# Optimization experiments

Measured on AMD Instinct MI355X. Metric: run time of the kernel, lower is better.

## Reference

```python
import jax, jax.numpy as jnp
import numpy as np

EPS = 1e-5

@jax.custom_vjp
def spike(u):
    return (u >= 0).astype(u.dtype)

def _spike_fwd(u):
    return spike(u), u

def _spike_bwd(u, g):
    return (g / (1.0 + 5.0 * jnp.abs(u)) ** 2,)

spike.defvjp(_spike_fwd, _spike_bwd)


def setup_inputs() -> dict:
    key = jax.random.key(0)
    ks = jax.random.split(key, 20)
    B, T, IN, TH, H = 2048, 320, 64, 128, 64
    d = {}
    d['x'] = jax.random.normal(ks[0], (B, T, IN), jnp.float32)
    d['tda'] = jax.random.normal(ks[1], (B, 150), jnp.float32)
    # depthwise conv: Conv1d(64,128,k=15,pad=7,groups=64) -> kernel [128, 1, 15]
    d['conv_w'] = jax.random.normal(ks[2], (TH, 1, 15), jnp.float32) * 0.1
    d['conv_b'] = jnp.zeros((TH,), jnp.float32)
    d['bn1_g'] = jnp.ones((TH,), jnp.float32)
    d['bn1_b'] = jnp.zeros((TH,), jnp.float32)
    d['bn1_m'] = jnp.zeros((TH,), jnp.float32)
    d['bn1_v'] = jnp.ones((TH,), jnp.float32)
    # spatial_fc: Linear(128,64), init mean=0.05 std=0.1
    d['sp_w'] = 0.05 + 0.1 * jax.random.normal(ks[3], (H, TH), jnp.float32)
    d['sp_b'] = jnp.zeros((H,), jnp.float32)
    d['li_w'] = jax.random.normal(ks[4], (H, 2 * H), jnp.float32) * (1.0 / np.sqrt(2 * H))
    d['li_b'] = jnp.zeros((H,), jnp.float32)
    d['tda_w1'] = jax.random.normal(ks[5], (64, 150), jnp.float32) * (1.0 / np.sqrt(150))
    d['tda_b1'] = jnp.zeros((64,), jnp.float32)
    d['tda_w2'] = jax.random.normal(ks[6], (32, 64), jnp.float32) * 0.125
    d['tda_b2'] = jnp.zeros((32,), jnp.float32)
    dp_out = (320 // 32) * H  # 640
    d['cls_w1'] = jax.random.normal(ks[7], (128, dp_out + 32), jnp.float32) * (1.0 / np.sqrt(dp_out + 32))
    d['cls_b1'] = jnp.zeros((128,), jnp.float32)
    d['bn2_g'] = jnp.ones((128,), jnp.float32)
    d['bn2_b'] = jnp.zeros((128,), jnp.float32)
    d['bn2_m'] = jnp.zeros((128,), jnp.float32)
    d['bn2_v'] = jnp.ones((128,), jnp.float32)
    d['cls_w2'] = jax.random.normal(ks[8], (4, 128), jnp.float32) * (1.0 / np.sqrt(128))
    d['cls_b2'] = jnp.zeros((4,), jnp.float32)
    return d


def reference(x, tda, conv_w, conv_b, bn1_g, bn1_b, bn1_m, bn1_v, sp_w, sp_b,
              li_w, li_b, tda_w1, tda_b1, tda_w2, tda_b2,
              cls_w1, cls_b1, bn2_g, bn2_b, bn2_m, bn2_v, cls_w2, cls_b2):
    B, T, _ = x.shape
    L_DP, N_DP, H = 32, 16, 64
    # temp_conv (eval mode: no dropout, BN with running stats)
    xc = jnp.transpose(x, (0, 2, 1))  # [B, 64, T]
    y = jax.lax.conv_general_dilated(
        xc, conv_w, window_strides=(1,), padding=[(7, 7)],
        dimension_numbers=('NCH', 'OIH', 'NCH'), feature_group_count=64)
    y = y + conv_b[None, :, None]
    y = (y - bn1_m[None, :, None]) * jax.lax.rsqrt(bn1_v + EPS)[None, :, None] * bn1_g[None, :, None] + bn1_b[None, :, None]
    y = jax.nn.relu(y)
    y = jnp.transpose(y, (0, 2, 1))  # [B, T, 128]
    # precompute all input currents: [T, B, 64] (time-major for scan)
    cur_all = jnp.einsum('bth,oh->tbo', y, sp_w) + sp_b

    def step(carry, cur):
        mf, ms, ml = carry
        mf = 0.5 * mf + cur
        sf = spike(mf - 0.5)
        mf = mf * (1.0 - sf)
        ms = 0.9 * ms + cur
        ss = spike(ms - 1.0)
        ms = ms * (1.0 - ss)
        cur_li = jnp.concatenate([sf, ss], axis=-1) @ li_w.T + li_b
        ml = 0.9 * ml + cur_li
        return (mf, ms, ml), ml

    z0 = jnp.zeros((B, H), x.dtype)
    _, li_seq = jax.lax.scan(step, (z0, z0, z0), cur_all)  # [T, B, 64]
    li_seq = jnp.transpose(li_seq, (1, 0, 2))  # [B, T, 64]

    windows = li_seq.reshape(B, T // L_DP, L_DP, H)
    start_mean = windows[:, :, :N_DP, :].mean(axis=2)
    end_mean = windows[:, :, -N_DP:, :].mean(axis=2)
    dp_feat = (end_mean - start_mean).reshape(B, -1)  # [B, 640]

    t1 = jax.nn.relu(tda @ tda_w1.T + tda_b1)
    tda_feat = jax.nn.relu(t1 @ tda_w2.T + tda_b2)  # [B, 32]

    h = jnp.concatenate([dp_feat, tda_feat], axis=-1) @ cls_w1.T + cls_b1
    h = (h - bn2_m) * jax.lax.rsqrt(bn2_v + EPS) * bn2_g + bn2_b
    h = jax.nn.relu(h)
    return h @ cls_w2.T + cls_b2  # [B, 4]
```

## Files before the change

### kernel.cpp

```cpp
#include <hip/hip_runtime.h>

#define NT 256

#define WS_SPWT    0
#define WS_SC1     8192
#define WS_SH1     8320
#define WS_SC2     8448
#define WS_SH2     8576
#define WS_LIWT    8704
#define WS_TW1T    16896
#define WS_TW2T    26496
#define WS_CW1T    28544
#define WS_TOTAL   114560
#define WS_WG      114560
#define WS_WBASE   114688
#define WS_CURBASE (114688 + 2048*1280)
#define CUR_STRIDE 20480

__global__ void prep_kernel(
    const float* __restrict__ conv_b, const float* __restrict__ bn1_g,
    const float* __restrict__ bn1_b,  const float* __restrict__ bn1_m,
    const float* __restrict__ bn1_v,  const float* __restrict__ sp_w,
    const float* __restrict__ li_w,   const float* __restrict__ tda_w1,
    const float* __restrict__ tda_w2, const float* __restrict__ cls_w1,
    const float* __restrict__ bn2_g,  const float* __restrict__ bn2_b,
    const float* __restrict__ bn2_m,  const float* __restrict__ bn2_v,
    float* __restrict__ ws)
{
    int i = blockIdx.x * NT + threadIdx.x;
    if (i > WS_TOTAL) return;
    if (i == WS_TOTAL) {
        float g = 0.f, sE = 0.f, sL = 0.f; int w = 0;
        for (int t = 0; t < 320; ++t) {
            g = fmaf(0.9f, g, 1.f);
            int pos = t & 31;
            if (pos < 16) sE += g; else sL += g;
            if (pos == 31) { ws[WS_WG + w] = sL - sE; ++w; sE = 0.f; sL = 0.f; }
        }
        return;
    }
    if (i < WS_SC1) {
        int c = i >> 6, h = i & 63;
        ws[i] = sp_w[h*128 + c];
    } else if (i < WS_SH1) {
        int c = i - WS_SC1;
        float vv = bn1_v[c] + 1e-5f;
        ws[i] = (float)((double)bn1_g[c] / sqrt((double)vv));
    } else if (i < WS_SC2) {
        int c = i - WS_SH1;
        float vv = bn1_v[c] + 1e-5f;
        double s = (double)bn1_g[c] / sqrt((double)vv);
        ws[i] = (float)(((double)conv_b[c] - (double)bn1_m[c])*s + (double)bn1_b[c]);
    } else if (i < WS_SH2) {
        int c = i - WS_SC2;
        float vv = bn2_v[c] + 1e-5f;
        ws[i] = (float)((double)bn2_g[c] / sqrt((double)vv));
    } else if (i < WS_LIWT) {
        int c = i - WS_SH2;
        float vv = bn2_v[c] + 1e-5f;
        double s = (double)bn2_g[c] / sqrt((double)vv);
        ws[i] = (float)((double)bn2_b[c] - (double)bn2_m[c]*s);
    } else if (i < WS_TW1T) {
        int t = i - WS_LIWT; int j = t >> 6, o = t & 63;
        ws[i] = li_w[o*128 + j];
    } else if (i < WS_TW2T) {
        int t = i - WS_TW1T; int r = t >> 6, o = t & 63;
        ws[i] = tda_w1[o*150 + r];
    } else if (i < WS_CW1T) {
        int t = i - WS_TW2T; int j = t >> 5, o = t & 31;
        ws[i] = tda_w2[o*64 + j];
    } else {
        int t = i - WS_CW1T; int j = t >> 7, c = t & 127;
        ws[i] = cls_w1[c*672 + j];
    }
}

__launch_bounds__(NT, 4)
__global__ void convproj_kernel(
    const float* __restrict__ x, const float* __restrict__ conv_w,
    const float* __restrict__ sp_b, const float* __restrict__ ws,
    float* __restrict__ cur, int b0)
{
    __shared__ float y_lds[128*65];

    const int tid = threadIdx.x;
    const int bi  = blockIdx.x;
    const int ic  = tid & 63;
    const int tg  = tid >> 6;
    const int lane = tid & 63;
    const int h0 = __builtin_amdgcn_readfirstlane((tid >> 6) << 4);

    float w0[15], w1[15];
    #pragma unroll
    for (int k = 0; k < 15; ++k) {
        w0[k] = conv_w[(2*ic)*15 + k];
        w1[k] = conv_w[(2*ic + 1)*15 + k];
    }
    const float sA = ws[WS_SC1 + 2*ic],     hA = ws[WS_SH1 + 2*ic];
    const float sB = ws[WS_SC1 + 2*ic + 1], hB = ws[WS_SH1 + 2*ic + 1];
    const float4* bp = reinterpret_cast<const float4*>(sp_b + h0);
    const float4 b0v = bp[0], b1v = bp[1], b2v = bp[2], b3v = bp[3];

    const float* __restrict__ spwT = ws;
    const float* xb = x + (size_t)(b0 + bi) * 20480 + ic;
    float* curb = cur + (size_t)bi * CUR_STRIDE;

    float xr0[30], xr1[30];
    #pragma unroll
    for (int r = 0; r < 30; ++r) {
        int t = tg*16 - 7 + r;
        xr0[r] = (t >= 0) ? xb[(size_t)t * 64] : 0.f;
    }

    #pragma unroll
    for (int chk = 0; chk < 5; ++chk) {
        float* xc = (chk & 1) ? xr1 : xr0;
        float* xn = (chk & 1) ? xr0 : xr1;

        #pragma unroll
        for (int j = 0; j < 16; ++j) {
            float a0 = 0.f, a1 = 0.f;
            #pragma unroll
            for (int k = 0; k < 15; ++k) {
                a0 = fmaf(xc[j + k], w0[k], a0);
                a1 = fmaf(xc[j + k], w1[k], a1);
            }
            int tt = tg*16 + j;
            y_lds[(2*ic)*65 + tt]     = fmaxf(fmaf(a0, sA, hA), 0.f);
            y_lds[(2*ic + 1)*65 + tt] = fmaxf(fmaf(a1, sB, hB), 0.f);
        }
        __syncthreads();

        if (chk < 4) {
            const int tbase = (chk + 1)*64 + tg*16 - 7;
            if (tbase + 29 < 320) {
                #pragma unroll
                for (int r = 0; r < 30; ++r)
                    xn[r] = xb[(size_t)(tbase + r) * 64];
            } else {
                #pragma unroll
                for (int r = 0; r < 30; ++r) {
                    int t = tbase + r;
                    xn[r] = (t < 320) ? xb[(size_t)t * 64] : 0.f;
                }
            }
        }

        {
            float acc[16];
            acc[0]=b0v.x;  acc[1]=b0v.y;  acc[2]=b0v.z;  acc[3]=b0v.w;
            acc[4]=b1v.x;  acc[5]=b1v.y;  acc[6]=b1v.z;  acc[7]=b1v.w;
            acc[8]=b2v.x;  acc[9]=b2v.y;  acc[10]=b2v.z; acc[11]=b2v.w;
            acc[12]=b3v.x; acc[13]=b3v.y; acc[14]=b3v.z; acc[15]=b3v.w;

            #pragma unroll 4
            for (int c = 0; c < 128; ++c) {
                float yv = y_lds[c*65 + lane];
                const float4* wp = reinterpret_cast<const float4*>(spwT + c*64 + h0);
                float4 q0 = wp[0], q1 = wp[1], q2 = wp[2], q3 = wp[3];
                acc[0]  = fmaf(yv, q0.x, acc[0]);
                acc[1]  = fmaf(yv, q0.y, acc[1]);
                acc[2]  = fmaf(yv, q0.z, acc[2]);
                acc[3]  = fmaf(yv, q0.w, acc[3]);
                acc[4]  = fmaf(yv, q1.x, acc[4]);
                acc[5]  = fmaf(yv, q1.y, acc[5]);
                acc[6]  = fmaf(yv, q1.z, acc[6]);
                acc[7]  = fmaf(yv, q1.w, acc[7]);
                acc[8]  = fmaf(yv, q2.x, acc[8]);
                acc[9]  = fmaf(yv, q2.y, acc[9]);
                acc[10] = fmaf(yv, q2.z, acc[10]);
                acc[11] = fmaf(yv, q2.w, acc[11]);
                acc[12] = fmaf(yv, q3.x, acc[12]);
                acc[13] = fmaf(yv, q3.y, acc[13]);
                acc[14] = fmaf(yv, q3.z, acc[14]);
                acc[15] = fmaf(yv, q3.w, acc[15]);
            }
            float* cb = curb + (size_t)h0 * 320 + chk*64 + lane;
            #pragma unroll
            for (int j = 0; j < 16; ++j)
                cb[(size_t)j*320] = acc[j];
        }
        __syncthreads();
    }
}

__device__ __forceinline__ void lif16(float4 n0, float4 n1, float4 n2, float4 n3,
    float& mf, float& ms, float& rlo, float& rhi,
    float& slo, float& shi)
{
    float v[16] = {n0.x,n0.y,n0.z,n0.w, n1.x,n1.y,n1.z,n1.w,
                   n2.x,n2.y,n2.z,n2.w, n3.x,n3.y,n3.z,n3.w};
    slo = 0.f; shi = 0.f;
    #pragma unroll
    for (int q = 0; q < 16; ++q) {
        float c = v[q];
        mf = fmaf(0.5f, mf, c);
        bool sf = mf >= 0.5f;
        ms = fmaf(0.9f, ms, c);
        bool ss = ms >= 1.0f;
        mf = sf ? 0.f : mf;
        ms = ss ? 0.f : ms;
        rlo = fmaf(0.9f, rlo, sf ? 1.f : 0.f);
        rhi = fmaf(0.9f, rhi, ss ? 1.f : 0.f);
        slo += rlo; shi += rhi;
    }
}

__global__ void scan_kernel(const float* __restrict__ cur,
                            float* __restrict__ W, int b0, int nb)
{
    const int wv = (int)((blockIdx.x * (unsigned)blockDim.x + threadIdx.x) >> 6);
    if (wv >= nb) return;
    const int lane = threadIdx.x & 63;
    const float* cb = cur + (size_t)wv * CUR_STRIDE + (size_t)lane * 320;
    float* Wb = W + (size_t)(b0 + wv) * 1280;

    float mf = 0.f, ms = 0.f, rlo = 0.f, rhi = 0.f;

    float4 A0 = *reinterpret_cast<const float4*>(cb);
    float4 A1 = *reinterpret_cast<const float4*>(cb + 4);
    float4 A2 = *reinterpret_cast<const float4*>(cb + 8);
    float4 A3 = *reinterpret_cast<const float4*>(cb + 12);
    float4 B0 = *reinterpret_cast<const float4*>(cb + 16);
    float4 B1 = *reinterpret_cast<const float4*>(cb + 20);
    float4 B2 = *reinterpret_cast<const float4*>(cb + 24);
    float4 B3 = *reinterpret_cast<const float4*>(cb + 28);

    #pragma unroll 1
    for (int tb = 0; tb < 20; tb += 2) {
        float sE_lo, sE_hi, slo, shi;
        lif16(A0, A1, A2, A3, mf, ms, rlo, rhi, sE_lo, sE_hi);
        if (tb + 2 < 20) {
            const float* p = cb + (tb + 2) * 16;
            A0 = *reinterpret_cast<const float4*>(p);
            A1 = *reinterpret_cast<const float4*>(p + 4);
            A2 = *reinterpret_cast<const float4*>(p + 8);
            A3 = *reinterpret_cast<const float4*>(p + 12);
        }
        lif16(B0, B1, B2, B3, mf, ms, rlo, rhi, slo, shi);
        if (tb + 3 < 20) {
            const float* p = cb + (tb + 3) * 16;
            B0 = *reinterpret_cast<const float4*>(p);
            B1 = *reinterpret_cast<const float4*>(p + 4);
            B2 = *reinterpret_cast<const float4*>(p + 8);
            B3 = *reinterpret_cast<const float4*>(p + 12);
        }
        int wdx = tb >> 1;
        Wb[wdx*128 + lane]      = slo - sE_lo;
        Wb[wdx*128 + 64 + lane] = shi - sE_hi;
    }
}

__global__ void epilogue_kernel(
    const float* __restrict__ tda,    const float* __restrict__ li_b,
    const float* __restrict__ tda_b1, const float* __restrict__ tda_b2,
    const float* __restrict__ cls_b1, const float* __restrict__ cls_w2,
    const float* __restrict__ cls_b2, const float* __restrict__ ws,
    const float* __restrict__ W,      float* __restrict__ out)
{
    __shared__ float Wl[1280];
    __shared__ float t1[64], tf[32], dp[640], h1[128];
    const int b = blockIdx.x, tid = threadIdx.x;

    for (int i = tid; i < 1280; i += NT)
        Wl[i] = W[(size_t)b*1280 + i];
    __syncthreads();

    const float* __restrict__ liwT = ws + WS_LIWT;
    const float* __restrict__ tw1T = ws + WS_TW1T;
    const float* __restrict__ tw2T = ws + WS_TW2T;
    const float* __restrict__ cw1T = ws + WS_CW1T;
    const float* tdab = tda + b*150;

    if (tid < 64) {
        float acc = tda_b1[tid];
        for (int i2 = 0; i2 < 150; ++i2)
            acc = fmaf(tdab[i2], tw1T[i2*64 + tid], acc);
        t1[tid] = fmaxf(acc, 0.f);
    }
    __syncthreads();
    if (tid < 32) {
        float acc = tda_b2[tid];
        #pragma unroll 8
        for (int j = 0; j < 64; ++j)
            acc = fmaf(t1[j], tw2T[j*32 + tid], acc);
        tf[tid] = fmaxf(acc, 0.f);
    }
    {
        int o = tid & 63;
        for (int w = tid >> 6; w < 10; w += 4) {
            float acc = li_b[o] * ws[WS_WG + w];
            #pragma unroll 4
            for (int j = 0; j < 128; ++j)
                acc = fmaf(Wl[w*128 + j], liwT[j*64 + o], acc);
            dp[w*64 + o] = 0.0625f * acc;
        }
    }
    __syncthreads();
    if (tid < 128) {
        float acc = cls_b1[tid];
        for (int j = 0; j < 640; ++j)
            acc = fmaf(dp[j], cw1T[j*128 + tid], acc);
        #pragma unroll 4
        for (int j = 0; j < 32; ++j)
            acc = fmaf(tf[j], cw1T[(640 + j)*128 + tid], acc);
        float s2 = ws[WS_SC2 + tid], sh2 = ws[WS_SH2 + tid];
        h1[tid] = fmaxf(fmaf(acc, s2, sh2), 0.f);
    }
    __syncthreads();
    if (tid < 4) {
        float acc = cls_b2[tid];
        for (int c = 0; c < 128; ++c)
            acc = fmaf(h1[c], cls_w2[tid*128 + c], acc);
        out[b*4 + tid] = acc;
    }
}

extern "C" void kernel_launch(void* const* d_in, const int* in_sizes, int n_in,
                              void* d_out, int out_size, void* d_ws, size_t ws_size,
                              hipStream_t stream) {
    const float* x      = (const float*)d_in[0];
    const float* tda    = (const float*)d_in[1];
    const float* conv_w = (const float*)d_in[2];
    const float* conv_b = (const float*)d_in[3];
    const float* bn1_g  = (const float*)d_in[4];
    const float* bn1_b  = (const float*)d_in[5];
    const float* bn1_m  = (const float*)d_in[6];
    const float* bn1_v  = (const float*)d_in[7];
    const float* sp_w   = (const float*)d_in[8];
    const float* sp_b   = (const float*)d_in[9];
    const float* li_w   = (const float*)d_in[10];
    const float* li_b   = (const float*)d_in[11];
    const float* tda_w1 = (const float*)d_in[12];
    const float* tda_b1 = (const float*)d_in[13];
    const float* tda_w2 = (const float*)d_in[14];
    const float* tda_b2 = (const float*)d_in[15];
    const float* cls_w1 = (const float*)d_in[16];
    const float* cls_b1 = (const float*)d_in[17];
    const float* bn2_g  = (const float*)d_in[18];
    const float* bn2_b  = (const float*)d_in[19];
    const float* bn2_m  = (const float*)d_in[20];
    const float* bn2_v  = (const float*)d_in[21];
    const float* cls_w2 = (const float*)d_in[22];
    const float* cls_b2 = (const float*)d_in[23];
    float* ws  = (float*)d_ws;
    float* out = (float*)d_out;

    const int B = in_sizes[0] / (320 * 64);

    prep_kernel<<<(WS_TOTAL + 1 + NT - 1)/NT, NT, 0, stream>>>(
        conv_b, bn1_g, bn1_b, bn1_m, bn1_v, sp_w,
        li_w, tda_w1, tda_w2, cls_w1,
        bn2_g, bn2_b, bn2_m, bn2_v, ws);

    long cap = (long)(ws_size / 4) - (long)WS_CURBASE;
    int nbg = (int)(cap / CUR_STRIDE);
    if (nbg < 1) nbg = 1;
    if (nbg > B) nbg = B;

    for (int g0 = 0; g0 < B; g0 += nbg) {
        int nb = (B - g0 < nbg) ? (B - g0) : nbg;
        convproj_kernel<<<nb, NT, 0, stream>>>(
            x, conv_w, sp_b, ws, ws + WS_CURBASE, g0);
        scan_kernel<<<(nb + 3)/4, NT, 0, stream>>>(
            ws + WS_CURBASE, ws + WS_WBASE, g0, nb);
    }

    epilogue_kernel<<<B, NT, 0, stream>>>(
        tda, li_b, tda_b1, tda_b2, cls_b1, cls_w2, cls_b2,
        ws, ws + WS_WBASE, out);
}
```

Before: 289.9 us.

## Fuse conv-projection and LIF scan into one kernel via LDS staging

Merges the conv/projection kernel and the scan kernel into a single per-batch kernel. Spatial currents are staged through a swizzled LDS buffer instead of a global workspace, and one wavefront runs the LIF recurrence on each 64-step chunk. The conv for the next chunk is reordered so the other waves can compute it while that wavefront scans. This removes the global round trip of the current tensor and the batch-group launch loop. The costs are more LDS per block, lower occupancy (launch bounds lowered from 4 to 3) and a serial scan on one wave inside the block, which may leave the other waves idle at the barrier.

Result: faster. 249.7 us (-13.8%).

```diff
diff --git a/kernel.cpp b/kernel.cpp
--- a/kernel.cpp
+++ b/kernel.cpp
@@ -14,8 +14,6 @@
 #define WS_TOTAL   114560
 #define WS_WG      114560
 #define WS_WBASE   114688
-#define WS_CURBASE (114688 + 2048*1280)
-#define CUR_STRIDE 20480
 
 __global__ void prep_kernel(
     const float* __restrict__ conv_b, const float* __restrict__ bn1_g,
@@ -75,20 +73,21 @@
     }
 }
 
-__launch_bounds__(NT, 4)
-__global__ void convproj_kernel(
+__launch_bounds__(NT, 3)
+__global__ void fused_kernel(
     const float* __restrict__ x, const float* __restrict__ conv_w,
     const float* __restrict__ sp_b, const float* __restrict__ ws,
-    float* __restrict__ cur, int b0)
+    float* __restrict__ wfeat)
 {
     __shared__ float y_lds[128*65];
-
-    const int tid = threadIdx.x;
-    const int bi  = blockIdx.x;
-    const int ic  = tid & 63;
-    const int tg  = tid >> 6;
+    __shared__ float cur_lds[64*64];
+
+    const int tid  = threadIdx.x;
+    const int b    = blockIdx.x;
+    const int ic   = tid & 63;
+    const int tg   = tid >> 6;
     const int lane = tid & 63;
-    const int h0 = __builtin_amdgcn_readfirstlane((tid >> 6) << 4);
+    const int h0   = __builtin_amdgcn_readfirstlane((tid >> 6) << 4);
 
     float w0[15], w1[15];
     #pragma unroll
@@ -102,8 +101,10 @@
     const float4 b0v = bp[0], b1v = bp[1], b2v = bp[2], b3v = bp[3];
 
     const float* __restrict__ spwT = ws;
-    const float* xb = x + (size_t)(b0 + bi) * 20480 + ic;
-    float* curb = cur + (size_t)bi * CUR_STRIDE;
+    const float* xb = x + (size_t)b * 20480 + ic;
+    float* Wb = wfeat + (size_t)b * 1280;
+
+    float mf = 0.f, ms = 0.f, rlo = 0.f, rhi = 0.f;
 
     float xr0[30], xr1[30];
     #pragma unroll
@@ -111,25 +112,23 @@
         int t = tg*16 - 7 + r;
         xr0[r] = (t >= 0) ? xb[(size_t)t * 64] : 0.f;
     }
+    #pragma unroll
+    for (int j = 0; j < 16; ++j) {
+        float a0 = 0.f, a1 = 0.f;
+        #pragma unroll
+        for (int k = 0; k < 15; ++k) {
+            a0 = fmaf(xr0[j + k], w0[k], a0);
+            a1 = fmaf(xr0[j + k], w1[k], a1);
+        }
+        int tt = tg*16 + j;
+        y_lds[(2*ic)*65 + tt]     = fmaxf(fmaf(a0, sA, hA), 0.f);
+        y_lds[(2*ic + 1)*65 + tt] = fmaxf(fmaf(a1, sB, hB), 0.f);
+    }
+    __syncthreads();
 
     #pragma unroll
     for (int chk = 0; chk < 5; ++chk) {
-        float* xc = (chk & 1) ? xr1 : xr0;
         float* xn = (chk & 1) ? xr0 : xr1;
-
-        #pragma unroll
-        for (int j = 0; j < 16; ++j) {
-            float a0 = 0.f, a1 = 0.f;
-            #pragma unroll
-            for (int k = 0; k < 15; ++k) {
-                a0 = fmaf(xc[j + k], w0[k], a0);
-                a1 = fmaf(xc[j + k], w1[k], a1);
-            }
-            int tt = tg*16 + j;
-            y_lds[(2*ic)*65 + tt]     = fmaxf(fmaf(a0, sA, hA), 0.f);
-            y_lds[(2*ic + 1)*65 + tt] = fmaxf(fmaf(a1, sB, hB), 0.f);
-        }
-        __syncthreads();
 
         if (chk < 4) {
             const int tbase = (chk + 1)*64 + tg*16 - 7;
@@ -175,79 +174,63 @@
                 acc[14] = fmaf(yv, q3.z, acc[14]);
                 acc[15] = fmaf(yv, q3.w, acc[15]);
             }
-            float* cb = curb + (size_t)h0 * 320 + chk*64 + lane;
+            const int tsw = (lane & 15) << 2;
             #pragma unroll
-            for (int j = 0; j < 16; ++j)
-                cb[(size_t)j*320] = acc[j];
+            for (int k = 0; k < 4; ++k) {
+                float4 v4 = make_float4(acc[4*k], acc[4*k+1], acc[4*k+2], acc[4*k+3]);
+                *reinterpret_cast<float4*>(&cur_lds[lane*64 + ((h0 + 4*k) ^ tsw)]) = v4;
+            }
         }
         __syncthreads();
-    }
-}
-
-__device__ __forceinline__ void lif16(float4 n0, float4 n1, float4 n2, float4 n3,
-    float& mf, float& ms, float& rlo, float& rhi,
-    float& slo, float& shi)
-{
-    float v[16] = {n0.x,n0.y,n0.z,n0.w, n1.x,n1.y,n1.z,n1.w,
-                   n2.x,n2.y,n2.z,n2.w, n3.x,n3.y,n3.z,n3.w};
-    slo = 0.f; shi = 0.f;
-    #pragma unroll
-    for (int q = 0; q < 16; ++q) {
-        float c = v[q];
-        mf = fmaf(0.5f, mf, c);
-        bool sf = mf >= 0.5f;
-        ms = fmaf(0.9f, ms, c);
-        bool ss = ms >= 1.0f;
-        mf = sf ? 0.f : mf;
-        ms = ss ? 0.f : ms;
-        rlo = fmaf(0.9f, rlo, sf ? 1.f : 0.f);
-        rhi = fmaf(0.9f, rhi, ss ? 1.f : 0.f);
-        slo += rlo; shi += rhi;
-    }
-}
-
-__global__ void scan_kernel(const float* __restrict__ cur,
-                            float* __restrict__ W, int b0, int nb)
-{
-    const int wv = (int)((blockIdx.x * (unsigned)blockDim.x + threadIdx.x) >> 6);
-    if (wv >= nb) return;
-    const int lane = threadIdx.x & 63;
-    const float* cb = cur + (size_t)wv * CUR_STRIDE + (size_t)lane * 320;
-    float* Wb = W + (size_t)(b0 + wv) * 1280;
-
-    float mf = 0.f, ms = 0.f, rlo = 0.f, rhi = 0.f;
-
-    float4 A0 = *reinterpret_cast<const float4*>(cb);
-    float4 A1 = *reinterpret_cast<const float4*>(cb + 4);
-    float4 A2 = *reinterpret_cast<const float4*>(cb + 8);
-    float4 A3 = *reinterpret_cast<const float4*>(cb + 12);
-    float4 B0 = *reinterpret_cast<const float4*>(cb + 16);
-    float4 B1 = *reinterpret_cast<const float4*>(cb + 20);
-    float4 B2 = *reinterpret_cast<const float4*>(cb + 24);
-    float4 B3 = *reinterpret_cast<const float4*>(cb + 28);
-
-    #pragma unroll 1
-    for (int tb = 0; tb < 20; tb += 2) {
-        float sE_lo, sE_hi, slo, shi;
-        lif16(A0, A1, A2, A3, mf, ms, rlo, rhi, sE_lo, sE_hi);
-        if (tb + 2 < 20) {
-            const float* p = cb + (tb + 2) * 16;
-            A0 = *reinterpret_cast<const float4*>(p);
-            A1 = *reinterpret_cast<const float4*>(p + 4);
-            A2 = *reinterpret_cast<const float4*>(p + 8);
-            A3 = *reinterpret_cast<const float4*>(p + 12);
-        }
-        lif16(B0, B1, B2, B3, mf, ms, rlo, rhi, slo, shi);
-        if (tb + 3 < 20) {
-            const float* p = cb + (tb + 3) * 16;
-            B0 = *reinterpret_cast<const float4*>(p);
-            B1 = *reinterpret_cast<const float4*>(p + 4);
-            B2 = *reinterpret_cast<const float4*>(p + 8);
-            B3 = *reinterpret_cast<const float4*>(p + 12);
-        }
-        int wdx = tb >> 1;
-        Wb[wdx*128 + lane]      = slo - sE_lo;
-        Wb[wdx*128 + 64 + lane] = shi - sE_hi;
+
+        if (tid < 64) {
+            float sE_lo = 0.f, sE_hi = 0.f;
+            #pragma unroll
+            for (int gq = 0; gq < 4; ++gq) {
+                float v[16];
+                #pragma unroll
+                for (int q = 0; q < 16; ++q) {
+                    int t = gq*16 + q;
+                    v[q] = cur_lds[t*64 + (lane ^ ((t & 15) << 2))];
+                }
+                float slo = 0.f, shi = 0.f;
+                #pragma unroll
+                for (int q = 0; q < 16; ++q) {
+                    float c = v[q];
+                    mf = fmaf(0.5f, mf, c);
+                    bool sf = mf >= 0.5f;
+                    ms = fmaf(0.9f, ms, c);
+                    bool ss = ms >= 1.0f;
+                    mf = sf ? 0.f : mf;
+                    ms = ss ? 0.f : ms;
+                    rlo = fmaf(0.9f, rlo, sf ? 1.f : 0.f);
+                    rhi = fmaf(0.9f, rhi, ss ? 1.f : 0.f);
+                    slo += rlo; shi += rhi;
+                }
+                if ((gq & 1) == 0) {
+                    sE_lo = slo; sE_hi = shi;
+                } else {
+                    int wdx = chk*2 + (gq >> 1);
+                    Wb[wdx*128 + lane]      = slo - sE_lo;
+                    Wb[wdx*128 + 64 + lane] = shi - sE_hi;
+                }
+            }
+        }
+        if (chk < 4) {
+            #pragma unroll
+            for (int j = 0; j < 16; ++j) {
+                float a0 = 0.f, a1 = 0.f;
+                #pragma unroll
+                for (int k = 0; k < 15; ++k) {
+                    a0 = fmaf(xn[j + k], w0[k], a0);
+                    a1 = fmaf(xn[j + k], w1[k], a1);
+                }
+                int tt = tg*16 + j;
+                y_lds[(2*ic)*65 + tt]     = fmaxf(fmaf(a0, sA, hA), 0.f);
+                y_lds[(2*ic + 1)*65 + tt] = fmaxf(fmaf(a1, sB, hB), 0.f);
+            }
+        }
+        __syncthreads();
     }
 }
 
@@ -353,18 +336,8 @@
         li_w, tda_w1, tda_w2, cls_w1,
         bn2_g, bn2_b, bn2_m, bn2_v, ws);
 
-    long cap = (long)(ws_size / 4) - (long)WS_CURBASE;
-    int nbg = (int)(cap / CUR_STRIDE);
-    if (nbg < 1) nbg = 1;
-    if (nbg > B) nbg = B;
-
-    for (int g0 = 0; g0 < B; g0 += nbg) {
-        int nb = (B - g0 < nbg) ? (B - g0) : nbg;
-        convproj_kernel<<<nb, NT, 0, stream>>>(
-            x, conv_w, sp_b, ws, ws + WS_CURBASE, g0);
-        scan_kernel<<<(nb + 3)/4, NT, 0, stream>>>(
-            ws + WS_CURBASE, ws + WS_WBASE, g0, nb);
-    }
+    fused_kernel<<<B, NT, 0, stream>>>(
+        x, conv_w, sp_b, ws, ws + WS_WBASE);
 
     epilogue_kernel<<<B, NT, 0, stream>>>(
         tda, li_b, tda_b1, tda_b2, cls_b1, cls_w2, cls_b2,
```
